# Kernel tuning notes

Hardware: AMD Instinct MI355X
Metric: run time of the kernel (lower is better)

The kernel has to match this reference:

```python
import jax, jax.numpy as jnp
import numpy as np

KM_ITERS = 20  # fixed Lloyd iterations (scipy kmeans iterates to tolerance with random init;
               # we use deterministic min/max init so centroid 0 = dark, 1 = bright)


def _kmeans_mask(img2d):
    """2-means clustering of pixel intensities of one [H,W] image + border-vote flip."""
    H, W = img2d.shape
    x = img2d.reshape(-1)  # [N]
    c0 = jnp.stack([x.min(), x.max()])  # deterministic init: centroid0=min, centroid1=max

    def step(c, _):
        code = jnp.argmin(jnp.abs(x[:, None] - c[None, :]), axis=1)  # [N] in {0,1}
        one = code == 1
        n1 = jnp.sum(one)
        n0 = x.shape[0] - n1
        s1 = jnp.sum(jnp.where(one, x, jnp.zeros_like(x)))
        s0 = jnp.sum(x) - s1
        c_new = jnp.stack([s0 / jnp.maximum(n0, 1).astype(x.dtype),
                           s1 / jnp.maximum(n1, 1).astype(x.dtype)])
        return c_new, None

    c, _ = jax.lax.scan(step, c0, None, length=KM_ITERS)
    # final assignment (scipy vq step)
    code = jnp.argmin(jnp.abs(x[:, None] - c[None, :]), axis=1).reshape(H, W)

    # border vote: if >=3 borders are mostly cluster-1, flip so text region is 1
    fc = code[:, 0].sum()
    lc = code[:, -1].sum()
    fr = code[0, :].sum()
    lr = code[-1, :].sum()
    num = ((fr > W // 2).astype(jnp.int32) + (lr > W // 2).astype(jnp.int32)
           + (fc > H // 2).astype(jnp.int32) + (lc > H // 2).astype(jnp.int32))
    mask = jnp.where(num >= 3, 1 - code, code)
    return mask.astype(img2d.dtype)


def get_mask(img_tensor):
    gray = img_tensor.mean(axis=1)  # [B,H,W]
    # clustering is non-differentiable in the original (runs on detached CPU numpy)
    masks = jax.vmap(_kmeans_mask)(jax.lax.stop_gradient(gray))
    return masks[:, None, :, :]  # [B,1,H,W]


def setup_inputs() -> dict:
    key = jax.random.key(0)
    k1, k2 = jax.random.split(key)
    B, C, H, W = 128, 3, 256, 256
    hr_img = jax.random.uniform(k1, (B, C, H, W), dtype=jnp.float32)
    sr_mask = jax.random.uniform(k2, (B, 1, H, W), dtype=jnp.float32)
    return {"hr_img": hr_img, "sr_mask": sr_mask}


def reference(hr_img, sr_mask):
    hr_mask = get_mask(hr_img)  # same spatial size -> no interpolation branch
    return jnp.mean((sr_mask - hr_mask) ** 2)
```

## Files before the change

### kernel.cpp

```cpp
#include <hip/hip_runtime.h>


constexpr int NB   = 2048;
constexpr int NPIX = 65536;
constexpr int KM_ITERS = 20;

constexpr size_t OFF_MINENC = 0;
constexpr size_t OFF_MAXBIT = 512;
constexpr size_t OFF_TINFO  = 1024;
constexpr size_t OFF_HCNT   = 4096;
constexpr size_t OFF_HSUM   = OFF_HCNT + (size_t)128 * NB * 4;
constexpr size_t OFF_BSUM   = OFF_HSUM + (size_t)128 * NB * 4;
constexpr size_t MEMSET_BYTES = OFF_BSUM;

__device__ __forceinline__ float waveSum(float v) {
#pragma unroll
    for (int off = 32; off > 0; off >>= 1) v += __shfl_down(v, off, 64);
    return v;
}
__device__ __forceinline__ float waveMin(float v) {
#pragma unroll
    for (int off = 32; off > 0; off >>= 1) v = fminf(v, __shfl_down(v, off, 64));
    return v;
}
__device__ __forceinline__ float waveMax(float v) {
#pragma unroll
    for (int off = 32; off > 0; off >>= 1) v = fmaxf(v, __shfl_down(v, off, 64));
    return v;
}

__global__ __launch_bounds__(256) void kA_hist(
        const float* __restrict__ hr, unsigned* __restrict__ minenc,
        unsigned* __restrict__ maxbits, unsigned* __restrict__ hcnt,
        float* __restrict__ hsum) {
    const int img = blockIdx.x >> 3, part = blockIdx.x & 7, tid = threadIdx.x;
    const int lane = tid & 63, wid = tid >> 6;

    __shared__ unsigned hcL[NB];
    __shared__ float    hsL[NB];
    __shared__ float    smn[4], smx[4];
    for (int j = tid; j < NB; j += 256) { hcL[j] = 0u; hsL[j] = 0.0f; }
    __syncthreads();

    const float* r = hr + (size_t)img * 3 * NPIX;
    const float* g = r + NPIX;
    const float* b = g + NPIX;

    float mn = 1e30f, mx = -1e30f;
#pragma unroll
    for (int i = 0; i < 8; ++i) {
        const int p = part * 8192 + i * 1024 + tid * 4;
        float4 rr = *(const float4*)(r + p);
        float4 gg = *(const float4*)(g + p);
        float4 bb = *(const float4*)(b + p);
        float x[4] = { (rr.x + gg.x + bb.x) * (1.0f / 3.0f),
                       (rr.y + gg.y + bb.y) * (1.0f / 3.0f),
                       (rr.z + gg.z + bb.z) * (1.0f / 3.0f),
                       (rr.w + gg.w + bb.w) * (1.0f / 3.0f) };
#pragma unroll
        for (int j = 0; j < 4; ++j) {
            mn = fminf(mn, x[j]); mx = fmaxf(mx, x[j]);
            int k = (int)(x[j] * (float)NB);
            k = max(0, min(NB - 1, k));
            atomicAdd(&hcL[k], 1u);
            atomicAdd(&hsL[k], x[j]);
        }
    }
    __syncthreads();

    for (int j = tid; j < NB; j += 256) {
        unsigned c = hcL[j];
        if (c) {
            atomicAdd(&hcnt[(size_t)img * NB + j], c);
            unsafeAtomicAdd(&hsum[(size_t)img * NB + j], hsL[j]);
        }
    }

    mn = waveMin(mn); mx = waveMax(mx);
    if (lane == 0) { smn[wid] = mn; smx[wid] = mx; }
    __syncthreads();
    if (tid == 0) {
        float bmn = fminf(fminf(smn[0], smn[1]), fminf(smn[2], smn[3]));
        float bmx = fmaxf(fmaxf(smx[0], smx[1]), fmaxf(smx[2], smx[3]));
        atomicMax(&maxbits[img], __float_as_uint(bmx));
        atomicMax(&minenc[img], 0xFFFFFFFFu - __float_as_uint(bmn));
    }
}

__global__ __launch_bounds__(256) void kB_lloyd(
        const unsigned* __restrict__ minenc, const unsigned* __restrict__ maxbits,
        const unsigned* __restrict__ hcnt, const float* __restrict__ hsum,
        float4* __restrict__ tinfo) {
    const int img = blockIdx.x, tid = threadIdx.x;
    __shared__ float sN[NB + 1], sS[NB + 1];
    __shared__ float tN[256], tS[256];

    const int base = tid * 8;
    float n8[8], s8[8];
#pragma unroll
    for (int u = 0; u < 8; ++u) {
        n8[u] = (float)hcnt[(size_t)img * NB + base + u];
        s8[u] = hsum[(size_t)img * NB + base + u];
    }
    float accN = 0.0f, accS = 0.0f;
#pragma unroll
    for (int u = 7; u >= 0; --u) {
        accN += n8[u]; n8[u] = accN;
        accS += s8[u]; s8[u] = accS;
    }
    tN[tid] = accN; tS[tid] = accS;
    __syncthreads();
    for (int off = 1; off < 256; off <<= 1) {
        float aN = 0.0f, aS = 0.0f;
        if (tid + off < 256) { aN = tN[tid + off]; aS = tS[tid + off]; }
        __syncthreads();
        tN[tid] += aN; tS[tid] += aS;
        __syncthreads();
    }
    const float exN = (tid < 255) ? tN[tid + 1] : 0.0f;
    const float exS = (tid < 255) ? tS[tid + 1] : 0.0f;
#pragma unroll
    for (int u = 0; u < 8; ++u) { sN[base + u] = n8[u] + exN; sS[base + u] = s8[u] + exS; }
    if (tid == 0) { sN[NB] = 0.0f; sS[NB] = 0.0f; }
    __syncthreads();

    if (tid == 0) {
        const float mn = __uint_as_float(0xFFFFFFFFu - minenc[img]);
        const float mx = __uint_as_float(maxbits[img]);
        const float Stot = sS[0];
        const float Ntot = (float)NPIX;
        float c0 = mn, c1 = mx;
#pragma unroll 1
        for (int it = 0; it < KM_ITERS; ++it) {
            const float t = 0.5f * (c0 + c1);
            float n1, s1;
            if (c1 == c0) { n1 = 0.0f; s1 = 0.0f; }
            else {
                const float f = t * (float)NB;
                int k = (int)floorf(f);
                k = max(0, min(NB - 1, k));
                float frac = (float)(k + 1) - f;
                frac = fminf(fmaxf(frac, 0.0f), 1.0f);
                const float cntk = sN[k] - sN[k + 1];
                const float sumk = sS[k] - sS[k + 1];
                const float aN = sN[k + 1] + cntk * frac;
                const float aS = sS[k + 1] + sumk * frac;
                if (c1 > c0) { n1 = aN; s1 = aS; }
                else         { n1 = Ntot - aN; s1 = Stot - aS; }
            }
            const float c1n = s1 / fmaxf(n1, 1.0f);
            const float c0n = (Stot - s1) / fmaxf(Ntot - n1, 1.0f);
            if (c1n == c1 && c0n == c0) break;
            c0 = c0n; c1 = c1n;
        }
        float tf, hii;
        if (c1 == c0) { tf = -1e30f; hii = 0.0f; }
        else { tf = 0.5f * (c0 + c1); hii = (c1 > c0) ? 1.0f : 0.0f; }
        tinfo[img] = make_float4(tf, hii, 0.0f, 0.0f);
    }
}

__global__ __launch_bounds__(256) void kC_border(
        const float* __restrict__ hr, float4* __restrict__ tinfo) {
    const int img = blockIdx.x, tid = threadIdx.x;
    const int lane = tid & 63, wid = tid >> 6;
    __shared__ float4 sm[4];

    const float4 ti = tinfo[img];
    const float t = ti.x;
    const bool hi = (ti.y != 0.0f);

    const float* r = hr + (size_t)img * 3 * NPIX;
    const float* g = r + NPIX;
    const float* b = g + NPIX;

    auto codeAt = [&](int p) -> float {
        const float x = (r[p] + g[p] + b[p]) * (1.0f / 3.0f);
        const bool one = hi ? (x > t) : (x < t);
        return one ? 1.0f : 0.0f;
    };
    float fr = codeAt(tid);
    float lr = codeAt(255 * 256 + tid);
    float fc = codeAt(tid * 256);
    float lc = codeAt(tid * 256 + 255);

    fr = waveSum(fr); lr = waveSum(lr); fc = waveSum(fc); lc = waveSum(lc);
    if (lane == 0) sm[wid] = make_float4(fr, lr, fc, lc);
    __syncthreads();
    if (tid == 0) {
        float FR = sm[0].x + sm[1].x + sm[2].x + sm[3].x;
        float LR = sm[0].y + sm[1].y + sm[2].y + sm[3].y;
        float FC = sm[0].z + sm[1].z + sm[2].z + sm[3].z;
        float LC = sm[0].w + sm[1].w + sm[2].w + sm[3].w;
        const int num = (FR > 128.0f) + (LR > 128.0f) + (FC > 128.0f) + (LC > 128.0f);
        tinfo[img].z = (num >= 3) ? 1.0f : 0.0f;
    }
}

__global__ __launch_bounds__(256) void kD_mse(
        const float* __restrict__ hr, const float* __restrict__ sr,
        const float4* __restrict__ tinfo, float* __restrict__ bsum) {
    const int img = blockIdx.x >> 3, part = blockIdx.x & 7, tid = threadIdx.x;
    const int lane = tid & 63, wid = tid >> 6;
    __shared__ float sm[4];

    const float4 ti = tinfo[img];
    const float t = ti.x;
    const bool hi   = (ti.y != 0.0f);
    const bool flip = (ti.z != 0.0f);

    const float* r = hr + (size_t)img * 3 * NPIX;
    const float* g = r + NPIX;
    const float* b = g + NPIX;
    const float* s = sr + (size_t)img * NPIX;

    float acc = 0.0f;
#pragma unroll
    for (int i = 0; i < 8; ++i) {
        const int p = part * 8192 + i * 1024 + tid * 4;
        float4 rr = *(const float4*)(r + p);
        float4 gg = *(const float4*)(g + p);
        float4 bb = *(const float4*)(b + p);
        float4 ss = *(const float4*)(s + p);
        float x[4] = { (rr.x + gg.x + bb.x) * (1.0f / 3.0f),
                       (rr.y + gg.y + bb.y) * (1.0f / 3.0f),
                       (rr.z + gg.z + bb.z) * (1.0f / 3.0f),
                       (rr.w + gg.w + bb.w) * (1.0f / 3.0f) };
        float sv[4] = { ss.x, ss.y, ss.z, ss.w };
#pragma unroll
        for (int j = 0; j < 4; ++j) {
            const bool one = hi ? (x[j] > t) : (x[j] < t);
            const float m = (one != flip) ? 1.0f : 0.0f;
            const float d = sv[j] - m;
            acc += d * d;
        }
    }
    acc = waveSum(acc);
    if (lane == 0) sm[wid] = acc;
    __syncthreads();
    if (tid == 0) bsum[blockIdx.x] = sm[0] + sm[1] + sm[2] + sm[3];
}

__global__ __launch_bounds__(256) void kE_final(
        const float* __restrict__ bsum, float* __restrict__ out) {
    const int tid = threadIdx.x, lane = tid & 63, wid = tid >> 6;
    __shared__ float sm[4];
    float v = bsum[tid] + bsum[tid + 256] + bsum[tid + 512] + bsum[tid + 768];
    v = waveSum(v);
    if (lane == 0) sm[wid] = v;
    __syncthreads();
    if (tid == 0) out[0] = (sm[0] + sm[1] + sm[2] + sm[3]) * (1.0f / 8388608.0f);
}

extern "C" void kernel_launch(void* const* d_in, const int* in_sizes, int n_in,
                              void* d_out, int out_size, void* d_ws, size_t ws_size,
                              hipStream_t stream) {
    const float* hr = (const float*)d_in[0];
    const float* sr = (const float*)d_in[1];
    float* out = (float*)d_out;

    char* ws = (char*)d_ws;
    unsigned* minenc  = (unsigned*)(ws + OFF_MINENC);
    unsigned* maxbits = (unsigned*)(ws + OFF_MAXBIT);
    float4*   tinfo   = (float4*)(ws + OFF_TINFO);
    unsigned* hcnt    = (unsigned*)(ws + OFF_HCNT);
    float*    hsum    = (float*)(ws + OFF_HSUM);
    float*    bsum    = (float*)(ws + OFF_BSUM);

    hipMemsetAsync(d_ws, 0, MEMSET_BYTES, stream);
    kA_hist  <<<1024, 256, 0, stream>>>(hr, minenc, maxbits, hcnt, hsum);
    kB_lloyd <<< 128, 256, 0, stream>>>(minenc, maxbits, hcnt, hsum, tinfo);
    kC_border<<< 128, 256, 0, stream>>>(hr, tinfo);
    kD_mse   <<<1024, 256, 0, stream>>>(hr, sr, tinfo, bsum);
    kE_final <<<   1, 256, 0, stream>>>(bsum, out);
}
```

Before: 209.3 us.

## Quantize gray to 16-bit, drop sum histogram, fuse border vote into MSE pass

The histogram pass now writes a 16-bit quantized grayscale image to workspace, so the MSE pass reads 2 bytes per pixel instead of re-reading three float channels. The per-bin float sum histogram and its LDS float atomics are removed; bin sums are approximated from counts using bin centers. The border-vote kernel is folded into the MSE kernel, which accumulates both flip and no-flip errors and lets the final kernel pick one per image. This cuts one launch and most of the second RGB read, at the cost of quantizing intensities and approximating cluster sums, which could move thresholds near bin edges.

```diff
diff --git a/kernel.cpp b/kernel.cpp
--- a/kernel.cpp
+++ b/kernel.cpp
@@ -4,49 +4,52 @@
 constexpr int NB   = 2048;
 constexpr int NPIX = 65536;
 constexpr int KM_ITERS = 20;
+constexpr float QINV  = 1.0f / 65536.0f;
+constexpr float BINW  = 1.0f / 2048.0f;
 
 constexpr size_t OFF_MINENC = 0;
-constexpr size_t OFF_MAXBIT = 512;
+constexpr size_t OFF_MAXU   = 512;
 constexpr size_t OFF_TINFO  = 1024;
-constexpr size_t OFF_HCNT   = 4096;
-constexpr size_t OFF_HSUM   = OFF_HCNT + (size_t)128 * NB * 4;
-constexpr size_t OFF_BSUM   = OFF_HSUM + (size_t)128 * NB * 4;
-constexpr size_t MEMSET_BYTES = OFF_BSUM;
-
-__device__ __forceinline__ float waveSum(float v) {
+constexpr size_t OFF_BORD   = 3072;
+constexpr size_t OFF_HCNT   = 8192;
+constexpr size_t OFF_GRAY   = OFF_HCNT + (size_t)128 * NB * 4;
+constexpr size_t OFF_BSUM   = OFF_GRAY + (size_t)128 * NPIX * 2;
+constexpr size_t MEMSET_BYTES = OFF_GRAY;
+
+__device__ __forceinline__ float waveSumF(float v) {
 #pragma unroll
     for (int off = 32; off > 0; off >>= 1) v += __shfl_down(v, off, 64);
     return v;
 }
-__device__ __forceinline__ float waveMin(float v) {
-#pragma unroll
-    for (int off = 32; off > 0; off >>= 1) v = fminf(v, __shfl_down(v, off, 64));
+__device__ __forceinline__ unsigned waveMinU(unsigned v) {
+#pragma unroll
+    for (int off = 32; off > 0; off >>= 1) v = min(v, (unsigned)__shfl_down((int)v, off, 64));
     return v;
 }
-__device__ __forceinline__ float waveMax(float v) {
-#pragma unroll
-    for (int off = 32; off > 0; off >>= 1) v = fmaxf(v, __shfl_down(v, off, 64));
+__device__ __forceinline__ unsigned waveMaxU(unsigned v) {
+#pragma unroll
+    for (int off = 32; off > 0; off >>= 1) v = max(v, (unsigned)__shfl_down((int)v, off, 64));
     return v;
 }
 
 __global__ __launch_bounds__(256) void kA_hist(
         const float* __restrict__ hr, unsigned* __restrict__ minenc,
-        unsigned* __restrict__ maxbits, unsigned* __restrict__ hcnt,
-        float* __restrict__ hsum) {
+        unsigned* __restrict__ maxu, unsigned* __restrict__ hcnt,
+        ushort* __restrict__ gray) {
     const int img = blockIdx.x >> 3, part = blockIdx.x & 7, tid = threadIdx.x;
     const int lane = tid & 63, wid = tid >> 6;
 
     __shared__ unsigned hcL[NB];
-    __shared__ float    hsL[NB];
-    __shared__ float    smn[4], smx[4];
-    for (int j = tid; j < NB; j += 256) { hcL[j] = 0u; hsL[j] = 0.0f; }
+    __shared__ unsigned smn[4], smx[4];
+    for (int j = tid; j < NB; j += 256) hcL[j] = 0u;
     __syncthreads();
 
     const float* r = hr + (size_t)img * 3 * NPIX;
     const float* g = r + NPIX;
     const float* b = g + NPIX;
-
-    float mn = 1e30f, mx = -1e30f;
+    ushort* gp = gray + (size_t)img * NPIX;
+
+    unsigned umn = 65535u, umx = 0u;
 #pragma unroll
     for (int i = 0; i < 8; ++i) {
         const int p = part * 8192 + i * 1024 + tid * 4;
@@ -57,40 +60,41 @@
                        (rr.y + gg.y + bb.y) * (1.0f / 3.0f),
                        (rr.z + gg.z + bb.z) * (1.0f / 3.0f),
                        (rr.w + gg.w + bb.w) * (1.0f / 3.0f) };
+        unsigned u[4];
 #pragma unroll
         for (int j = 0; j < 4; ++j) {
-            mn = fminf(mn, x[j]); mx = fmaxf(mx, x[j]);
-            int k = (int)(x[j] * (float)NB);
-            k = max(0, min(NB - 1, k));
-            atomicAdd(&hcL[k], 1u);
-            atomicAdd(&hsL[k], x[j]);
+            unsigned uu = (unsigned)(x[j] * 65536.0f);
+            uu = min(uu, 65535u);
+            u[j] = uu;
+            umn = min(umn, uu); umx = max(umx, uu);
+            atomicAdd(&hcL[uu >> 5], 1u);
         }
+        ushort4 u4;
+        u4.x = (ushort)u[0]; u4.y = (ushort)u[1];
+        u4.z = (ushort)u[2]; u4.w = (ushort)u[3];
+        *(ushort4*)(gp + p) = u4;
     }
     __syncthreads();
 
     for (int j = tid; j < NB; j += 256) {
-        unsigned c = hcL[j];
-        if (c) {
-            atomicAdd(&hcnt[(size_t)img * NB + j], c);
-            unsafeAtomicAdd(&hsum[(size_t)img * NB + j], hsL[j]);
-        }
-    }
-
-    mn = waveMin(mn); mx = waveMax(mx);
-    if (lane == 0) { smn[wid] = mn; smx[wid] = mx; }
+        const unsigned c = hcL[j];
+        if (c) atomicAdd(&hcnt[(size_t)img * NB + j], c);
+    }
+
+    umn = waveMinU(umn); umx = waveMaxU(umx);
+    if (lane == 0) { smn[wid] = umn; smx[wid] = umx; }
     __syncthreads();
     if (tid == 0) {
-        float bmn = fminf(fminf(smn[0], smn[1]), fminf(smn[2], smn[3]));
-        float bmx = fmaxf(fmaxf(smx[0], smx[1]), fmaxf(smx[2], smx[3]));
-        atomicMax(&maxbits[img], __float_as_uint(bmx));
-        atomicMax(&minenc[img], 0xFFFFFFFFu - __float_as_uint(bmn));
+        const unsigned bmn = min(min(smn[0], smn[1]), min(smn[2], smn[3]));
+        const unsigned bmx = max(max(smx[0], smx[1]), max(smx[2], smx[3]));
+        atomicMax(&maxu[img], bmx);
+        atomicMax(&minenc[img], 65535u - bmn);
     }
 }
 
 __global__ __launch_bounds__(256) void kB_lloyd(
-        const unsigned* __restrict__ minenc, const unsigned* __restrict__ maxbits,
-        const unsigned* __restrict__ hcnt, const float* __restrict__ hsum,
-        float4* __restrict__ tinfo) {
+        const unsigned* __restrict__ minenc, const unsigned* __restrict__ maxu,
+        const unsigned* __restrict__ hcnt, float4* __restrict__ tinfo) {
     const int img = blockIdx.x, tid = threadIdx.x;
     __shared__ float sN[NB + 1], sS[NB + 1];
     __shared__ float tN[256], tS[256];
@@ -99,8 +103,9 @@
     float n8[8], s8[8];
 #pragma unroll
     for (int u = 0; u < 8; ++u) {
-        n8[u] = (float)hcnt[(size_t)img * NB + base + u];
-        s8[u] = hsum[(size_t)img * NB + base + u];
+        const float c = (float)hcnt[(size_t)img * NB + base + u];
+        n8[u] = c;
+        s8[u] = c * (((float)(base + u) + 0.484375f) * BINW);
     }
     float accN = 0.0f, accS = 0.0f;
 #pragma unroll
@@ -125,11 +130,10 @@
     __syncthreads();
 
     if (tid == 0) {
-        const float mn = __uint_as_float(0xFFFFFFFFu - minenc[img]);
-        const float mx = __uint_as_float(maxbits[img]);
+        float c0 = (float)(65535u - minenc[img]) * QINV;
+        float c1 = (float)maxu[img] * QINV;
         const float Stot = sS[0];
         const float Ntot = (float)NPIX;
-        float c0 = mn, c1 = mx;
 #pragma unroll 1
         for (int it = 0; it < KM_ITERS; ++it) {
             const float t = 0.5f * (c0 + c1);
@@ -142,9 +146,9 @@
                 float frac = (float)(k + 1) - f;
                 frac = fminf(fmaxf(frac, 0.0f), 1.0f);
                 const float cntk = sN[k] - sN[k + 1];
-                const float sumk = sS[k] - sS[k + 1];
                 const float aN = sN[k + 1] + cntk * frac;
-                const float aS = sS[k + 1] + sumk * frac;
+                const float aS = sS[k + 1] +
+                                 cntk * frac * 0.5f * (t + (float)(k + 1) * BINW);
                 if (c1 > c0) { n1 = aN; s1 = aS; }
                 else         { n1 = Ntot - aN; s1 = Stot - aS; }
             }
@@ -160,94 +164,88 @@
     }
 }
 
-__global__ __launch_bounds__(256) void kC_border(
-        const float* __restrict__ hr, float4* __restrict__ tinfo) {
-    const int img = blockIdx.x, tid = threadIdx.x;
+__global__ __launch_bounds__(256) void kC_mse(
+        const ushort* __restrict__ gray, const float* __restrict__ sr,
+        const float4* __restrict__ tinfo, unsigned* __restrict__ bord,
+        float2* __restrict__ bsum) {
+    const int img = blockIdx.x >> 3, part = blockIdx.x & 7, tid = threadIdx.x;
     const int lane = tid & 63, wid = tid >> 6;
-    __shared__ float4 sm[4];
+    __shared__ float sA0[4], sA1[4];
+    __shared__ float4 sB[4];
 
     const float4 ti = tinfo[img];
     const float t = ti.x;
     const bool hi = (ti.y != 0.0f);
 
-    const float* r = hr + (size_t)img * 3 * NPIX;
-    const float* g = r + NPIX;
-    const float* b = g + NPIX;
-
-    auto codeAt = [&](int p) -> float {
-        const float x = (r[p] + g[p] + b[p]) * (1.0f / 3.0f);
-        const bool one = hi ? (x > t) : (x < t);
-        return one ? 1.0f : 0.0f;
-    };
-    float fr = codeAt(tid);
-    float lr = codeAt(255 * 256 + tid);
-    float fc = codeAt(tid * 256);
-    float lc = codeAt(tid * 256 + 255);
-
-    fr = waveSum(fr); lr = waveSum(lr); fc = waveSum(fc); lc = waveSum(lc);
-    if (lane == 0) sm[wid] = make_float4(fr, lr, fc, lc);
-    __syncthreads();
-    if (tid == 0) {
-        float FR = sm[0].x + sm[1].x + sm[2].x + sm[3].x;
-        float LR = sm[0].y + sm[1].y + sm[2].y + sm[3].y;
-        float FC = sm[0].z + sm[1].z + sm[2].z + sm[3].z;
-        float LC = sm[0].w + sm[1].w + sm[2].w + sm[3].w;
-        const int num = (FR > 128.0f) + (LR > 128.0f) + (FC > 128.0f) + (LC > 128.0f);
-        tinfo[img].z = (num >= 3) ? 1.0f : 0.0f;
-    }
-}
-
-__global__ __launch_bounds__(256) void kD_mse(
-        const float* __restrict__ hr, const float* __restrict__ sr,
-        const float4* __restrict__ tinfo, float* __restrict__ bsum) {
-    const int img = blockIdx.x >> 3, part = blockIdx.x & 7, tid = threadIdx.x;
-    const int lane = tid & 63, wid = tid >> 6;
-    __shared__ float sm[4];
-
-    const float4 ti = tinfo[img];
-    const float t = ti.x;
-    const bool hi   = (ti.y != 0.0f);
-    const bool flip = (ti.z != 0.0f);
-
-    const float* r = hr + (size_t)img * 3 * NPIX;
-    const float* g = r + NPIX;
-    const float* b = g + NPIX;
-    const float* s = sr + (size_t)img * NPIX;
-
-    float acc = 0.0f;
+    const ushort* gp = gray + (size_t)img * NPIX;
+    const float*  sp = sr   + (size_t)img * NPIX;
+
+    float a0 = 0.0f, a1 = 0.0f;
+    float fr = 0.0f, lr = 0.0f, fc = 0.0f, lc = 0.0f;
 #pragma unroll
     for (int i = 0; i < 8; ++i) {
         const int p = part * 8192 + i * 1024 + tid * 4;
-        float4 rr = *(const float4*)(r + p);
-        float4 gg = *(const float4*)(g + p);
-        float4 bb = *(const float4*)(b + p);
-        float4 ss = *(const float4*)(s + p);
-        float x[4] = { (rr.x + gg.x + bb.x) * (1.0f / 3.0f),
-                       (rr.y + gg.y + bb.y) * (1.0f / 3.0f),
-                       (rr.z + gg.z + bb.z) * (1.0f / 3.0f),
-                       (rr.w + gg.w + bb.w) * (1.0f / 3.0f) };
-        float sv[4] = { ss.x, ss.y, ss.z, ss.w };
+        ushort4 u4 = *(const ushort4*)(gp + p);
+        float4  ss = *(const float4*)(sp + p);
+        const unsigned uu[4] = { u4.x, u4.y, u4.z, u4.w };
+        const float    sv[4] = { ss.x, ss.y, ss.z, ss.w };
+        const int row = p >> 8;
 #pragma unroll
         for (int j = 0; j < 4; ++j) {
-            const bool one = hi ? (x[j] > t) : (x[j] < t);
-            const float m = (one != flip) ? 1.0f : 0.0f;
-            const float d = sv[j] - m;
-            acc += d * d;
+            const float x = (float)uu[j] * QINV;
+            const bool one = hi ? (x > t) : (x < t);
+            const float m = one ? 1.0f : 0.0f;
+            const float d0 = sv[j] - m;
+            const float d1 = sv[j] - (1.0f - m);
+            a0 += d0 * d0;
+            a1 += d1 * d1;
+            const int col = (p & 255) + j;
+            if (col == 0)   fc += m;
+            if (col == 255) lc += m;
+            if (row == 0)   fr += m;
+            if (row == 255) lr += m;
         }
     }
-    acc = waveSum(acc);
+    a0 = waveSumF(a0); a1 = waveSumF(a1);
+    fr = waveSumF(fr); lr = waveSumF(lr); fc = waveSumF(fc); lc = waveSumF(lc);
+    if (lane == 0) { sA0[wid] = a0; sA1[wid] = a1; sB[wid] = make_float4(fr, lr, fc, lc); }
+    __syncthreads();
+    if (tid == 0) {
+        bsum[blockIdx.x] = make_float2(sA0[0] + sA0[1] + sA0[2] + sA0[3],
+                                       sA1[0] + sA1[1] + sA1[2] + sA1[3]);
+        const float FR = sB[0].x + sB[1].x + sB[2].x + sB[3].x;
+        const float LR = sB[0].y + sB[1].y + sB[2].y + sB[3].y;
+        const float FC = sB[0].z + sB[1].z + sB[2].z + sB[3].z;
+        const float LC = sB[0].w + sB[1].w + sB[2].w + sB[3].w;
+        unsigned* bb = bord + (size_t)img * 4;
+        if (FR > 0.5f) atomicAdd(&bb[0], (unsigned)(FR + 0.5f));
+        if (LR > 0.5f) atomicAdd(&bb[1], (unsigned)(LR + 0.5f));
+        if (FC > 0.5f) atomicAdd(&bb[2], (unsigned)(FC + 0.5f));
+        if (LC > 0.5f) atomicAdd(&bb[3], (unsigned)(LC + 0.5f));
+    }
+}
+
+__global__ __launch_bounds__(256) void kD_final(
+        const unsigned* __restrict__ bord, const float2* __restrict__ bsum,
+        float* __restrict__ out) {
+    const int tid = threadIdx.x, lane = tid & 63, wid = tid >> 6;
+    __shared__ float flipS[128];
+    __shared__ float sm[4];
+    if (tid < 128) {
+        const unsigned* bb = bord + (size_t)tid * 4;
+        const int num = (bb[0] > 128u) + (bb[1] > 128u) + (bb[2] > 128u) + (bb[3] > 128u);
+        flipS[tid] = (num >= 3) ? 1.0f : 0.0f;
+    }
+    __syncthreads();
+    float acc = 0.0f;
+#pragma unroll
+    for (int q = 0; q < 4; ++q) {
+        const int e = tid * 4 + q;
+        const float2 v = bsum[e];
+        acc += (flipS[e >> 3] != 0.0f) ? v.y : v.x;
+    }
+    acc = waveSumF(acc);
     if (lane == 0) sm[wid] = acc;
-    __syncthreads();
-    if (tid == 0) bsum[blockIdx.x] = sm[0] + sm[1] + sm[2] + sm[3];
-}
-
-__global__ __launch_bounds__(256) void kE_final(
-        const float* __restrict__ bsum, float* __restrict__ out) {
-    const int tid = threadIdx.x, lane = tid & 63, wid = tid >> 6;
-    __shared__ float sm[4];
-    float v = bsum[tid] + bsum[tid + 256] + bsum[tid + 512] + bsum[tid + 768];
-    v = waveSum(v);
-    if (lane == 0) sm[wid] = v;
     __syncthreads();
     if (tid == 0) out[0] = (sm[0] + sm[1] + sm[2] + sm[3]) * (1.0f / 8388608.0f);
 }
@@ -260,17 +258,17 @@
     float* out = (float*)d_out;
 
     char* ws = (char*)d_ws;
-    unsigned* minenc  = (unsigned*)(ws + OFF_MINENC);
-    unsigned* maxbits = (unsigned*)(ws + OFF_MAXBIT);
-    float4*   tinfo   = (float4*)(ws + OFF_TINFO);
-    unsigned* hcnt    = (unsigned*)(ws + OFF_HCNT);
-    float*    hsum    = (float*)(ws + OFF_HSUM);
-    float*    bsum    = (float*)(ws + OFF_BSUM);
+    unsigned* minenc = (unsigned*)(ws + OFF_MINENC);
+    unsigned* maxu   = (unsigned*)(ws + OFF_MAXU);
+    float4*   tinfo  = (float4*)(ws + OFF_TINFO);
+    unsigned* bord   = (unsigned*)(ws + OFF_BORD);
+    unsigned* hcnt   = (unsigned*)(ws + OFF_HCNT);
+    ushort*   gray   = (ushort*)(ws + OFF_GRAY);
+    float2*   bsum   = (float2*)(ws + OFF_BSUM);
 
     hipMemsetAsync(d_ws, 0, MEMSET_BYTES, stream);
-    kA_hist  <<<1024, 256, 0, stream>>>(hr, minenc, maxbits, hcnt, hsum);
-    kB_lloyd <<< 128, 256, 0, stream>>>(minenc, maxbits, hcnt, hsum, tinfo);
-    kC_border<<< 128, 256, 0, stream>>>(hr, tinfo);
-    kD_mse   <<<1024, 256, 0, stream>>>(hr, sr, tinfo, bsum);
-    kE_final <<<   1, 256, 0, stream>>>(bsum, out);
-}
+    kA_hist <<<1024, 256, 0, stream>>>(hr, minenc, maxu, hcnt, gray);
+    kB_lloyd<<< 128, 256, 0, stream>>>(minenc, maxu, hcnt, tinfo);
+    kC_mse  <<<1024, 256, 0, stream>>>(gray, sr, tinfo, bord, bsum);
+    kD_final<<<   1, 256, 0, stream>>>(bord, bsum, out);
+}
```

Result: faster. 189.3 us (-9.6%).
